# Optimization experiments

Hardware: AMD Instinct MI355X
Metric: run time of the kernel (lower is better)

Reference implementation:

```python
import jax, jax.numpy as jnp
import numpy as np

B, IN, H, OUT = 131072, 16, 64, 16
STEPS = 30   # PCNet.inference default steps
LR = 0.1     # PCNet.inference default lr


def setup_inputs() -> dict:
    key = jax.random.key(0)
    ks = jax.random.split(key, 5)
    return {
        "x": jax.random.normal(ks[0], (B, IN), jnp.float32),
        "W1": jax.random.normal(ks[1], (H, IN), jnp.float32) * 0.1,
        "b1": jnp.zeros((H,), jnp.float32),
        "W2": jax.random.normal(ks[2], (OUT, H), jnp.float32) * 0.1,
        "b2": jnp.zeros((OUT,), jnp.float32),
        "x1_init": jax.random.normal(ks[3], (B, H), jnp.float32),
        "x2_init": jax.random.normal(ks[4], (B, OUT), jnp.float32),
    }


def reference(x, W1, b1, W2, b2, x1_init, x2_init):
    # mu1 = layer1(x) depends only on x -> constant across inference steps
    mu1 = jax.nn.sigmoid(x @ W1.T + b1)              # [B, H]

    def step(carry, _):
        x1, x2 = carry
        mu2 = jax.nn.sigmoid(x1 @ W2.T + b2)         # [B, OUT]
        e1 = x1 - mu1                                # [B, H]
        e2 = x2 - mu2                                # [B, OUT]
        # analytic grads of sum(e1^2) + sum(e2^2) w.r.t. x1, x2
        # (same values torch.autograd.grad produces in PCNet.inference)
        g1 = 2.0 * e1 - 2.0 * ((e2 * mu2 * (1.0 - mu2)) @ W2)
        g2 = 2.0 * e2
        return (x1 - LR * g1, x2 - LR * g2), None

    (x1, x2), _ = jax.lax.scan(step, (x1_init, x2_init), None, length=STEPS)
    return x1, x2
```

## Files before the change

kernel.cpp:

```cpp
#include <hip/hip_runtime.h>

#define NB 131072
#define NSTEPS 30
#define LAMBDA  1.2379400392853803e-3f
#define ONEMLAM 0.9987620599607146f

typedef float  float4v __attribute__((ext_vector_type(4)));
typedef short  short4v __attribute__((ext_vector_type(4)));

#define MFMA16 __builtin_amdgcn_mfma_f32_16x16x16bf16_1k

static __device__ __forceinline__ unsigned fb(float f) {
    union { float f; unsigned u; } c; c.f = f; return c.u;
}
static __device__ __forceinline__ float fu(unsigned u) {
    union { unsigned u; float f; } c; c.u = u; return c.f;
}

struct bfpair { short4v hi, lo; };

static __device__ __forceinline__ bfpair split4(float4v v) {
    unsigned u0 = fb(v[0]), u1 = fb(v[1]), u2 = fb(v[2]), u3 = fb(v[3]);
    float l0 = v[0] - fu(u0 & 0xffff0000u);
    float l1 = v[1] - fu(u1 & 0xffff0000u);
    float l2 = v[2] - fu(u2 & 0xffff0000u);
    float l3 = v[3] - fu(u3 & 0xffff0000u);
    union { unsigned u[2]; short4v s; } H, L;
    H.u[0] = __builtin_amdgcn_perm(u1, u0, 0x07060302u);
    H.u[1] = __builtin_amdgcn_perm(u3, u2, 0x07060302u);
    L.u[0] = __builtin_amdgcn_perm(fb(l1), fb(l0), 0x07060302u);
    L.u[1] = __builtin_amdgcn_perm(fb(l3), fb(l2), 0x07060302u);
    bfpair P; P.hi = H.s; P.lo = L.s; return P;
}

static __device__ __forceinline__ short4v pack_hi4(float4v v) {
    union { unsigned u[2]; short4v s; } H;
    H.u[0] = __builtin_amdgcn_perm(fb(v[1]), fb(v[0]), 0x07060302u);
    H.u[1] = __builtin_amdgcn_perm(fb(v[3]), fb(v[2]), 0x07060302u);
    return H.s;
}

static __device__ __forceinline__ float sigmoid_f(float p) {
    return __builtin_amdgcn_rcpf(1.0f + __expf(-p));
}

__global__ __launch_bounds__(256, 3) void pcnet_kernel(
    const float* __restrict__ x,
    const float* __restrict__ W1,
    const float* __restrict__ b1,
    const float* __restrict__ W2,
    const float* __restrict__ b2,
    const float* __restrict__ x1i,
    const float* __restrict__ x2i,
    float* __restrict__ out)
{
    const int tid  = blockIdx.x * 256 + threadIdx.x;
    const int wave = tid >> 6;
    const int lane = threadIdx.x & 63;
    const int g = lane >> 4;
    const int q = lane & 15;
    int rr[2];
    rr[0] = wave * 32 + q;
    rr[1] = rr[0] + 16;

    bfpair a_w2[4];
#pragma unroll
    for (int c = 0; c < 4; ++c) {
        float4v w = *(const float4v*)(W2 + q * 64 + 16 * c + 4 * g);
        a_w2[c] = split4(w);
    }
    const float4v b2f = *(const float4v*)(b2 + 4 * g);
    const float4v zero4 = {0.f, 0.f, 0.f, 0.f};

    bfpair bx[2];
#pragma unroll
    for (int i = 0; i < 2; ++i)
        bx[i] = split4(*(const float4v*)(x + rr[i] * 16 + 4 * g));

    float4v x1c[2][4];
    float4v pacc[2], cacc[2];
#pragma unroll
    for (int i = 0; i < 2; ++i) { pacc[i] = b2f; cacc[i] = zero4; }
#pragma unroll
    for (int t = 0; t < 4; ++t) {
        float4v aw = *(const float4v*)(W1 + (16 * t + q) * 16 + 4 * g);
        bfpair a1 = split4(aw);
        float4v binit = *(const float4v*)(b1 + 16 * t + 4 * g);
#pragma unroll
        for (int i = 0; i < 2; ++i) {
            float4v acc = binit;
            acc = MFMA16(a1.hi, bx[i].hi, acc, 0, 0, 0);
            acc = MFMA16(a1.hi, bx[i].lo, acc, 0, 0, 0);
            acc = MFMA16(a1.lo, bx[i].hi, acc, 0, 0, 0);
            float4v x10 = *(const float4v*)(x1i + rr[i] * 64 + 16 * t + 4 * g);
            float4v m;
#pragma unroll
            for (int j = 0; j < 4; ++j) m[j] = sigmoid_f(acc[j]);
#pragma unroll
            for (int j = 0; j < 4; ++j)
                x1c[i][t][j] = fmaf(LAMBDA, x10[j], ONEMLAM * m[j]);
            bfpair b1s = split4(x10);
            bfpair bm  = split4(m);
            pacc[i] = MFMA16(a_w2[t].hi, b1s.hi, pacc[i], 0, 0, 0);
            pacc[i] = MFMA16(a_w2[t].hi, b1s.lo, pacc[i], 0, 0, 0);
            pacc[i] = MFMA16(a_w2[t].lo, b1s.hi, pacc[i], 0, 0, 0);
            cacc[i] = MFMA16(a_w2[t].hi, bm.hi,  cacc[i], 0, 0, 0);
            cacc[i] = MFMA16(a_w2[t].hi, bm.lo,  cacc[i], 0, 0, 0);
            cacc[i] = MFMA16(a_w2[t].lo, bm.hi,  cacc[i], 0, 0, 0);
        }
    }
    float4v pv[2], qv[2];
#pragma unroll
    for (int i = 0; i < 2; ++i) {
        pv[i] = pacc[i];
#pragma unroll
        for (int j = 0; j < 4; ++j) qv[i][j] = 0.2f * (b2f[j] + cacc[i][j]);
    }

    float4v Ma = zero4, Mb = zero4, Mc = zero4;
#pragma unroll
    for (int c = 0; c < 4; ++c) {
        Ma = MFMA16(a_w2[c].hi, a_w2[c].hi, Ma, 0, 0, 0);
        Mb = MFMA16(a_w2[c].hi, a_w2[c].lo, Mb, 0, 0, 0);
        Mc = MFMA16(a_w2[c].lo, a_w2[c].hi, Mc, 0, 0, 0);
    }
    short4v mfr = pack_hi4(0.2f * ((Ma + Mb) + Mc));

    float4v x2v[2], Sv[2];
#pragma unroll
    for (int i = 0; i < 2; ++i) {
        x2v[i] = *(const float4v*)(x2i + rr[i] * 16 + 4 * g);
        Sv[i] = zero4;
    }

#pragma unroll 1
    for (int s = 0; s < NSTEPS; ++s) {
#pragma unroll
        for (int i = 0; i < 2; ++i) {
            float4v dv;
#pragma unroll
            for (int j = 0; j < 4; ++j) {
                float mu2 = sigmoid_f(pv[i][j]);
                float e2  = x2v[i][j] - mu2;
                float mm  = fmaf(-mu2, mu2, mu2);
                dv[j]  = e2 * mm;
                x2v[i][j] = fmaf(-0.2f, e2, x2v[i][j]);
                Sv[i][j]  = fmaf(0.8f, Sv[i][j], dv[j]);
            }
            short4v bd = pack_hi4(dv);
            float4v pn;
#pragma unroll
            for (int j = 0; j < 4; ++j) pn[j] = fmaf(0.8f, pv[i][j], qv[i][j]);
            pv[i] = MFMA16(mfr, bd, pn, 0, 0, 0);
        }
    }

    short4v bs[2];
#pragma unroll
    for (int i = 0; i < 2; ++i) bs[i] = pack_hi4(Sv[i]);
#pragma unroll
    for (int t = 0; t < 4; ++t) {
        float4v e;
        e[0] = 0.2f * W2[(4 * g + 0) * 64 + 16 * t + q];
        e[1] = 0.2f * W2[(4 * g + 1) * 64 + 16 * t + q];
        e[2] = 0.2f * W2[(4 * g + 2) * 64 + 16 * t + q];
        e[3] = 0.2f * W2[(4 * g + 3) * 64 + 16 * t + q];
        bfpair a_ep = split4(e);
#pragma unroll
        for (int i = 0; i < 2; ++i) {
            float4v acc = x1c[i][t];
            acc = MFMA16(a_ep.hi, bs[i], acc, 0, 0, 0);
            acc = MFMA16(a_ep.lo, bs[i], acc, 0, 0, 0);
            *(float4v*)(out + rr[i] * 64 + 16 * t + 4 * g) = acc;
        }
    }
#pragma unroll
    for (int i = 0; i < 2; ++i)
        *(float4v*)(out + (size_t)NB * 64 + rr[i] * 16 + 4 * g) = x2v[i];
}

extern "C" void kernel_launch(void* const* d_in, const int* in_sizes, int n_in,
                              void* d_out, int out_size, void* d_ws, size_t ws_size,
                              hipStream_t stream) {
    const float* x   = (const float*)d_in[0];
    const float* W1  = (const float*)d_in[1];
    const float* b1  = (const float*)d_in[2];
    const float* W2  = (const float*)d_in[3];
    const float* b2  = (const float*)d_in[4];
    const float* x1i = (const float*)d_in[5];
    const float* x2i = (const float*)d_in[6];
    float* out = (float*)d_out;

    dim3 grid(NB / 128);
    dim3 block(256);
    pcnet_kernel<<<grid, block, 0, stream>>>(x, W1, b1, W2, b2, x1i, x2i, out);
}
```

Baseline: 33.62 us.

## Drop bf16 split-precision terms in W2 projections and use one-wave blocks

The precompute of W2·x1 and W2·mu1 now uses a single bf16 hi×hi MFMA instead of the three-term hi/lo split, which cuts MFMA and packing work. Launch geometry changes from 256-thread blocks to 64-thread single-wave blocks with four times as many blocks. The step loop is rewritten in vector form, which is mostly cosmetic. The lower precision of the initial projection could push error past tolerance, since it feeds all 30 recurrence steps.

```diff
diff --git a/kernel.cpp b/kernel.cpp
--- a/kernel.cpp
+++ b/kernel.cpp
@@ -44,7 +44,7 @@
     return __builtin_amdgcn_rcpf(1.0f + __expf(-p));
 }
 
-__global__ __launch_bounds__(256, 3) void pcnet_kernel(
+__global__ __launch_bounds__(64, 4) void pcnet_kernel(
     const float* __restrict__ x,
     const float* __restrict__ W1,
     const float* __restrict__ b1,
@@ -54,13 +54,11 @@
     const float* __restrict__ x2i,
     float* __restrict__ out)
 {
-    const int tid  = blockIdx.x * 256 + threadIdx.x;
-    const int wave = tid >> 6;
     const int lane = threadIdx.x & 63;
     const int g = lane >> 4;
     const int q = lane & 15;
     int rr[2];
-    rr[0] = wave * 32 + q;
+    rr[0] = blockIdx.x * 32 + q;
     rr[1] = rr[0] + 16;
 
     bfpair a_w2[4];
@@ -96,25 +94,16 @@
             float4v m;
 #pragma unroll
             for (int j = 0; j < 4; ++j) m[j] = sigmoid_f(acc[j]);
-#pragma unroll
-            for (int j = 0; j < 4; ++j)
-                x1c[i][t][j] = fmaf(LAMBDA, x10[j], ONEMLAM * m[j]);
-            bfpair b1s = split4(x10);
-            bfpair bm  = split4(m);
-            pacc[i] = MFMA16(a_w2[t].hi, b1s.hi, pacc[i], 0, 0, 0);
-            pacc[i] = MFMA16(a_w2[t].hi, b1s.lo, pacc[i], 0, 0, 0);
-            pacc[i] = MFMA16(a_w2[t].lo, b1s.hi, pacc[i], 0, 0, 0);
-            cacc[i] = MFMA16(a_w2[t].hi, bm.hi,  cacc[i], 0, 0, 0);
-            cacc[i] = MFMA16(a_w2[t].hi, bm.lo,  cacc[i], 0, 0, 0);
-            cacc[i] = MFMA16(a_w2[t].lo, bm.hi,  cacc[i], 0, 0, 0);
+            x1c[i][t] = LAMBDA * x10 + ONEMLAM * m;
+            pacc[i] = MFMA16(a_w2[t].hi, pack_hi4(x10), pacc[i], 0, 0, 0);
+            cacc[i] = MFMA16(a_w2[t].hi, pack_hi4(m),   cacc[i], 0, 0, 0);
         }
     }
     float4v pv[2], qv[2];
 #pragma unroll
     for (int i = 0; i < 2; ++i) {
         pv[i] = pacc[i];
-#pragma unroll
-        for (int j = 0; j < 4; ++j) qv[i][j] = 0.2f * (b2f[j] + cacc[i][j]);
+        qv[i] = 0.2f * (b2f + cacc[i]);
     }
 
     float4v Ma = zero4, Mb = zero4, Mc = zero4;
@@ -137,21 +126,16 @@
     for (int s = 0; s < NSTEPS; ++s) {
 #pragma unroll
         for (int i = 0; i < 2; ++i) {
-            float4v dv;
+            float4v mu2;
 #pragma unroll
-            for (int j = 0; j < 4; ++j) {
-                float mu2 = sigmoid_f(pv[i][j]);
-                float e2  = x2v[i][j] - mu2;
-                float mm  = fmaf(-mu2, mu2, mu2);
-                dv[j]  = e2 * mm;
-                x2v[i][j] = fmaf(-0.2f, e2, x2v[i][j]);
-                Sv[i][j]  = fmaf(0.8f, Sv[i][j], dv[j]);
-            }
-            short4v bd = pack_hi4(dv);
-            float4v pn;
-#pragma unroll
-            for (int j = 0; j < 4; ++j) pn[j] = fmaf(0.8f, pv[i][j], qv[i][j]);
-            pv[i] = MFMA16(mfr, bd, pn, 0, 0, 0);
+            for (int j = 0; j < 4; ++j) mu2[j] = sigmoid_f(pv[i][j]);
+            float4v e2 = x2v[i] - mu2;
+            float4v mm = mu2 - mu2 * mu2;
+            float4v dv = e2 * mm;
+            x2v[i] = x2v[i] - 0.2f * e2;
+            Sv[i]  = 0.8f * Sv[i] + dv;
+            float4v pn = 0.8f * pv[i] + qv[i];
+            pv[i] = MFMA16(mfr, pack_hi4(dv), pn, 0, 0, 0);
         }
     }
 
@@ -191,7 +175,7 @@
     const float* x2i = (const float*)d_in[6];
     float* out = (float*)d_out;
 
-    dim3 grid(NB / 128);
-    dim3 block(256);
+    dim3 grid(NB / 32);
+    dim3 block(64);
     pcnet_kernel<<<grid, block, 0, stream>>>(x, W1, b1, W2, b2, x1i, x2i, out);
 }
```

Result: slower. 42.06 us (+25.1%).
